# Performance work log

Hardware: AMD Instinct MI355X
Metric: run time of the kernel (lower is better)

The kernel has to match this reference:

```python
import jax, jax.numpy as jnp
import numpy as np

B, N, L, C, K = 2, 8192, 8192, 128, 8
RADIUS = 0.4

def _gather(t, idx):
    # t: [B,L,D], idx: [B,N,K] -> [B,N,K,D]
    b, n, k = idx.shape
    return jnp.take_along_axis(t, idx.reshape(b, n * k)[:, :, None], axis=1).reshape(b, n, k, t.shape[-1])

def _ln(x, g, b):
    m = x.mean(-1, keepdims=True)
    v = x.var(-1, keepdims=True)
    return (x - m) * jax.lax.rsqrt(v + 1e-5) * g + b

def setup_inputs() -> dict:
    key = jax.random.key(0)
    ks = jax.random.split(key, 16)
    F = 4 * C
    def w(k, i, o):
        return jax.random.normal(k, (i, o), jnp.float32) / np.sqrt(i).astype(np.float32)
    return {
        "q_xyz": jax.random.uniform(ks[0], (B, N, 3), jnp.float32),
        "q_feat": jax.random.normal(ks[1], (B, N, C), jnp.float32),
        "kv_xyz": jax.random.uniform(ks[2], (B, L, 3), jnp.float32),
        "kv_feat": jax.random.normal(ks[3], (B, L, C), jnp.float32),
        "kv_pad": jnp.zeros((B, L), bool),
        "pos_w1": w(ks[4], 3, C), "pos_b1": jnp.zeros((C,), jnp.float32),
        "pos_w2": w(ks[5], C, C), "pos_b2": jnp.zeros((C,), jnp.float32),
        "attn_w": w(ks[6], C, C), "attn_b": jnp.zeros((C,), jnp.float32),
        "lin_w": w(ks[7], C, C),
        "lin_src_w": w(ks[8], C, C),
        "lin_dst_w": w(ks[9], C, C),
        "ln1_g": jnp.ones((C,), jnp.float32), "ln1_b": jnp.zeros((C,), jnp.float32),
        "ffn_w1": w(ks[10], C, F), "ffn_b1": jnp.zeros((F,), jnp.float32),
        "ffn_w2": w(ks[11], F, C), "ffn_b2": jnp.zeros((C,), jnp.float32),
        "ln2_g": jnp.ones((C,), jnp.float32), "ln2_b": jnp.zeros((C,), jnp.float32),
    }

def reference(q_xyz, q_feat, kv_xyz, kv_feat, kv_pad,
              pos_w1, pos_b1, pos_w2, pos_b2, attn_w, attn_b,
              lin_w, lin_src_w, lin_dst_w, ln1_g, ln1_b,
              ffn_w1, ffn_b1, ffn_w2, ffn_b2, ln2_g, ln2_b):
    # --- radius graph: up to K nearest kv points within RADIUS per query ---
    d2 = jnp.sum((q_xyz[:, :, None, :] - kv_xyz[:, None, :, :]) ** 2, -1)  # [B,N,L]
    ok = (d2 <= RADIUS ** 2) & (~kv_pad)[:, None, :]
    neg_d2, idx = jax.lax.top_k(jnp.where(ok, -d2, -jnp.inf), K)  # [B,N,K]
    ev = jnp.isfinite(neg_d2)  # edge-valid mask [B,N,K]

    # --- PointTransformerConv (vector attention, per-edge) ---
    pos_j = _gather(kv_xyz, idx)                           # [B,N,K,3]
    rel = q_xyz[:, :, None, :] - pos_j                     # pos_i - pos_j
    # pos_nn: MLP([3,C,C], plain_last=False) => ReLU after each Linear
    delta = jax.nn.relu(jax.nn.relu(rel @ pos_w1 + pos_b1) @ pos_w2 + pos_b2)  # [B,N,K,C]
    a_src = _gather(kv_feat @ lin_src_w, idx)              # [B,N,K,C]
    a_dst = q_feat @ lin_dst_w                             # [B,N,C]
    x_j = _gather(kv_feat @ lin_w, idx)                    # [B,N,K,C]
    # attn_nn: MLP([C,C], plain_last=False) => Linear + ReLU
    alpha = jax.nn.relu((a_dst[:, :, None, :] - a_src + delta) @ attn_w + attn_b)
    # segment softmax over the K neighbors (invalid edges masked out)
    scores = jnp.where(ev[..., None], alpha, -jnp.inf)
    mx = jnp.max(scores, axis=2, keepdims=True)
    mx = jnp.where(jnp.isfinite(mx), mx, 0.0)
    e = jnp.where(ev[..., None], jnp.exp(scores - mx), 0.0)
    attn = e / jnp.maximum(e.sum(2, keepdims=True), 1e-12)
    agg = jnp.sum(attn * (x_j + delta), axis=2)            # [B,N,C]

    # --- residual + LN + FFN + LN (dropout = identity at eval) ---
    out = _ln(q_feat + agg, ln1_g, ln1_b)
    h = jax.nn.gelu(out @ ffn_w1 + ffn_b1, approximate=False) @ ffn_w2 + ffn_b2
    return _ln(out + h, ln2_g, ln2_b)
```

## Files before the change

kernel.cpp:

```cpp
#include <hip/hip_runtime.h>
#include <math.h>

#define NB 2
#define NQ 8192
#define NL 8192
#define NC 128
#define NKN 8
#define NF 512
#define MQ (NB*NQ)

typedef __attribute__((ext_vector_type(8))) short bf16x8;
typedef __attribute__((ext_vector_type(4))) float f32x4;

__device__ __forceinline__ unsigned short f2bf_u(float f){
    unsigned u = __float_as_uint(f);
    return (unsigned short)((u + 0x7FFFu + ((u>>16)&1u)) >> 16);
}
__device__ __forceinline__ float bf2f(unsigned short s){
    return __uint_as_float(((unsigned)s) << 16);
}


__global__ __launch_bounds__(256) void grid_zero_kernel(int* __restrict__ p)
{
    int t = blockIdx.x*256 + threadIdx.x;
    p[t] = 0;
}

__device__ __forceinline__ int cell_coord(float x) {
    int c = (int)(x * 16.0f);
    return min(15, max(0, c));
}

__global__ __launch_bounds__(256) void grid_count_kernel(
    const float* __restrict__ kxyz, const unsigned char* __restrict__ pad,
    int* __restrict__ cnt)
{
    int t = blockIdx.x*256 + threadIdx.x;
    if (pad[t]) return;
    int bat = t >> 13;
    float x = kxyz[t*3+0], y = kxyz[t*3+1], z = kxyz[t*3+2];
    int cell = (cell_coord(z)*16 + cell_coord(y))*16 + cell_coord(x);
    atomicAdd(&cnt[bat*4096 + cell], 1);
}

__global__ __launch_bounds__(1024) void grid_scan_kernel(
    const int* __restrict__ cnt, int* __restrict__ cs)
{
    __shared__ int wsum[17];
    int t = threadIdx.x;
    int v[8]; int s = 0;
    #pragma unroll
    for (int k = 0; k < 8; ++k) { v[k] = s; s += cnt[t*8 + k]; }
    int lane = t & 63, w = t >> 6;
    int inc = s;
    #pragma unroll
    for (int d = 1; d < 64; d <<= 1) {
        int o = __shfl_up(inc, d);
        if (lane >= d) inc += o;
    }
    if (lane == 63) wsum[w] = inc;
    __syncthreads();
    if (t == 0) {
        int a = 0;
        for (int i = 0; i < 16; ++i) { int x = wsum[i]; wsum[i] = a; a += x; }
        wsum[16] = a;
    }
    __syncthreads();
    int base = wsum[w] + (inc - s);
    #pragma unroll
    for (int k = 0; k < 8; ++k) cs[t*8 + k] = base + v[k];
    if (t == 1023) cs[8192] = wsum[16];
}

__global__ __launch_bounds__(256) void grid_scatter_kernel(
    const float* __restrict__ kxyz, const unsigned char* __restrict__ pad,
    const int* __restrict__ cs, int* __restrict__ fill, float4* __restrict__ ro)
{
    int t = blockIdx.x*256 + threadIdx.x;
    if (pad[t]) return;
    int bat = t >> 13, i = t & 8191;
    float x = kxyz[t*3+0], y = kxyz[t*3+1], z = kxyz[t*3+2];
    int cell = bat*4096 + (cell_coord(z)*16 + cell_coord(y))*16 + cell_coord(x);
    int pos = cs[cell] + atomicAdd(&fill[cell], 1);
    ro[pos] = make_float4(x, y, z, __int_as_float(i));
}

__device__ __forceinline__ void insert8(float cd, int id, float dk[8], int ik[8]) {
    if (cd < dk[7]) {
        dk[7] = cd; ik[7] = id;
        #pragma unroll
        for (int r = 6; r >= 0; --r) {
            bool sw = dk[r+1] < dk[r];
            float td = dk[r]; int ti = ik[r];
            dk[r]   = sw ? dk[r+1] : dk[r];
            ik[r]   = sw ? ik[r+1] : ik[r];
            dk[r+1] = sw ? td : dk[r+1];
            ik[r+1] = sw ? ti : ik[r+1];
        }
    }
}

template<int W>
__device__ __forceinline__ void scan_block(int l, int cx, int cy, int cz,
    float qx, float qy, float qz, const int* __restrict__ CS,
    const float4* __restrict__ RO, float dk[8], int ik[8])
{
    const int D = 2*W + 1;
    int xs = max(0, cx - W), xe = min(15, cx + W);
    int nx = xe - xs + 1;
    for (int r = l; r < D*D; r += 8) {
        int dz = r / D - W, dy = r % D - W;
        int zz = cz + dz, yy = cy + dy;
        if ((unsigned)zz > 15u || (unsigned)yy > 15u) continue;
        int c0 = (zz*16 + yy)*16 + xs;
        int s = CS[c0], e = CS[c0 + nx];
        for (int p = s; p < e; ++p) {
            float4 v = RO[p];
            float dx = qx - v.x, dyv = qy - v.y, dzv = qz - v.z;
            float cd = dx*dx + dyv*dyv + dzv*dzv;
            insert8(cd, __float_as_int(v.w), dk, ik);
        }
    }
}

__device__ __forceinline__ void merge8(float dk[8], int ik[8]) {
    #pragma unroll
    for (int m = 1; m <= 4; m <<= 1) {
        float od[8]; int oi[8];
        #pragma unroll
        for (int r = 0; r < 8; ++r) {
            od[r] = __shfl_xor(dk[r], m);
            oi[r] = __shfl_xor(ik[r], m);
        }
        float nd[8]; int ni[8];
        #pragma unroll
        for (int r = 0; r < 8; ++r) {
            bool take = od[7-r] < dk[r];
            nd[r] = take ? od[7-r] : dk[r];
            ni[r] = take ? oi[7-r] : ik[r];
        }
        #pragma unroll
        for (int st = 4; st >= 1; st >>= 1) {
            #pragma unroll
            for (int r = 0; r < 8; ++r) {
                if ((r & st) == 0 && (r | st) < 8) {
                    int b = r | st;
                    bool sw = nd[b] < nd[r];
                    float td = nd[r]; int ti = ni[r];
                    nd[r] = sw ? nd[b] : nd[r];
                    ni[r] = sw ? ni[b] : ni[r];
                    nd[b] = sw ? td : nd[b];
                    ni[b] = sw ? ti : ni[b];
                }
            }
        }
        #pragma unroll
        for (int r = 0; r < 8; ++r) { dk[r] = nd[r]; ik[r] = ni[r]; }
    }
}

__global__ __launch_bounds__(256) void radius_grid_query_kernel(
    const float* __restrict__ qxyz, const int* __restrict__ cellstart,
    const float4* __restrict__ reorder, int* __restrict__ idxout)
{
    const int tid  = threadIdx.x;
    const int l    = tid & 7;
    const int qloc = tid >> 3;
    const int gq   = blockIdx.x*32 + qloc;
    const int bat  = gq >> 13;
    const float qx = qxyz[gq*3+0], qy = qxyz[gq*3+1], qz = qxyz[gq*3+2];
    const int cx = cell_coord(qx), cy = cell_coord(qy), cz = cell_coord(qz);
    const int* CS = cellstart + bat*4096;
    const float R2  = (float)(0.4*0.4);
    const float R2P = __uint_as_float(__float_as_uint(R2) + 1u);

    float dk[8]; int ik[8];
    #pragma unroll
    for (int r = 0; r < 8; ++r) { dk[r] = R2P; ik[r] = -1; }

    scan_block<2>(l, cx, cy, cz, qx, qy, qz, CS, reorder, dk, ik);
    merge8(dk, ik);
    bool done = dk[7] <= 0.015625f;

    if (!done) {
        #pragma unroll
        for (int r = 0; r < 8; ++r) { dk[r] = R2P; ik[r] = -1; }
        scan_block<4>(l, cx, cy, cz, qx, qy, qz, CS, reorder, dk, ik);
        merge8(dk, ik);
        done = dk[7] <= 0.0625f;
    }
    if (!done) {
        #pragma unroll
        for (int r = 0; r < 8; ++r) { dk[r] = R2P; ik[r] = -1; }
        scan_block<16>(l, cx, cy, cz, qx, qy, qz, CS, reorder, dk, ik);
        merge8(dk, ik);
    }

    if (l == 0) {
        int o[8];
        #pragma unroll
        for (int r = 0; r < 8; ++r) o[r] = (dk[r] <= R2) ? ik[r] : -1;
        int4 a = {o[0], o[1], o[2], o[3]};
        int4 b = {o[4], o[5], o[6], o[7]};
        *(int4*)&idxout[(size_t)gq*8 + 0] = a;
        *(int4*)&idxout[(size_t)gq*8 + 4] = b;
    }
}

__global__ __launch_bounds__(256) void prep_all_kernel(
    const float* __restrict__ posw2, const float* __restrict__ attnw,
    const float* __restrict__ lin_w, const float* __restrict__ lin_src_w,
    const float* __restrict__ lin_dst_w,
    const float* __restrict__ ffn_w1, const float* __restrict__ ffn_w2,
    unsigned short* __restrict__ imgb)
{
    int t = blockIdx.x*256 + threadIdx.x;
    if (t < 16384) {
        int k = t >> 7, n = t & 127;
        imgb[(k >> 5)*4096 + n*32 + (k & 31)] = f2bf_u(posw2[t]);
    } else if (t < 32768) {
        int u = t - 16384;
        int k = u >> 7, n = u & 127;
        imgb[16384 + (k >> 5)*4096 + n*32 + (k & 31)] = f2bf_u(attnw[u]);
    } else if (t < 65536) {
        int u = t - 32768;
        int k = u >> 8, n = u & 255;
        float v = (n < 128) ? lin_w[k*128 + n] : lin_src_w[k*128 + (n-128)];
        imgb[32768 + ((k >> 5)*256 + n)*32 + (k & 31)] = f2bf_u(v);
    } else if (t < 81920) {
        int u = t - 65536;
        int k = u >> 7, n = u & 127;
        imgb[65536 + ((k >> 5)*128 + n)*32 + (k & 31)] = f2bf_u(lin_dst_w[u]);
    } else if (t < 147456) {
        int u = t - 81920;
        int k = u >> 9, n = u & 511;
        imgb[81920 + ((k >> 5)*512 + n)*32 + (k & 31)] = f2bf_u(ffn_w1[u]);
    } else {
        int u = t - 147456;
        int k = u >> 7, n = u & 127;
        imgb[147456 + ((k >> 5)*128 + n)*32 + (k & 31)] = f2bf_u(ffn_w2[u]);
    }
}

__device__ inline float gelu_exact(float x) {
    return 0.5f*x*(1.0f + erff(x*0.7071067811865476f));
}

template<int ACT, bool OUTBF>
__global__ __launch_bounds__(256) void gemm_mfma(
    const float* __restrict__ A, const unsigned short* __restrict__ Bimg,
    const float* __restrict__ bias, void* __restrict__ outv,
    int Kd, int Nd)
{
    __shared__ unsigned short sA[64*32];
    __shared__ unsigned short sB[128*32];
    const int tid = threadIdx.x;
    const int w = tid >> 6, lane = tid & 63, l15 = lane & 15, quad = lane >> 4;
    const int row0 = blockIdx.x*64, col0 = blockIdx.y*128;

    f32x4 acc[8];
    #pragma unroll
    for (int t=0;t<8;t++){ acc[t][0]=0.f; acc[t][1]=0.f; acc[t][2]=0.f; acc[t][3]=0.f; }

    const int nch = Kd >> 5;
    for (int kc = 0; kc < nch; ++kc) {
        __syncthreads();
        #pragma unroll
        for (int it = 0; it < 2; ++it) {
            int idx = it*256 + tid;
            int r = idx >> 3, kq = idx & 7;
            float4 a4 = *(const float4*)&A[(size_t)(row0+r)*Kd + kc*32 + kq*4];
            ushort4 pk = { f2bf_u(a4.x), f2bf_u(a4.y), f2bf_u(a4.z), f2bf_u(a4.w) };
            *(ushort4*)&sA[r*32 + kq*4] = pk;
        }
        const int4* bsrc = (const int4*)(Bimg + ((size_t)kc*Nd + col0)*32);
        #pragma unroll
        for (int it = 0; it < 2; ++it) {
            int o = it*256 + tid;
            ((int4*)sB)[o] = bsrc[o];
        }
        __syncthreads();
        bf16x8 af = *(const bf16x8*)&sA[(w*16 + l15)*32 + quad*8];
        #pragma unroll
        for (int t = 0; t < 8; ++t) {
            bf16x8 bf = *(const bf16x8*)&sB[(16*t + l15)*32 + quad*8];
            acc[t] = __builtin_amdgcn_mfma_f32_16x16x32_bf16(af, bf, acc[t], 0, 0, 0);
        }
    }

    const int rowb = row0 + w*16 + quad*4;
    #pragma unroll
    for (int t = 0; t < 8; ++t) {
        int col = col0 + 16*t + l15;
        float bv = bias ? bias[col] : 0.f;
        #pragma unroll
        for (int r = 0; r < 4; ++r) {
            float x = acc[t][r] + bv;
            if (ACT == 1) x = gelu_exact(x);
            if (OUTBF) ((unsigned short*)outv)[(size_t)(rowb+r)*Nd + col] = f2bf_u(x);
            else       ((float*)outv)[(size_t)(rowb+r)*Nd + col] = x;
        }
    }
}

__global__ __launch_bounds__(256) void gemm2_ln_mfma(
    const unsigned short* __restrict__ Abf, const unsigned short* __restrict__ Bimg,
    const float* __restrict__ b2, const float* __restrict__ res,
    const float* __restrict__ g, const float* __restrict__ bb,
    float* __restrict__ out)
{
    __shared__ unsigned short sA[64*32];
    __shared__ unsigned short sB[128*32];
    const int tid = threadIdx.x;
    const int w = tid >> 6, lane = tid & 63, l15 = lane & 15, quad = lane >> 4;
    const int row0 = blockIdx.x*64;

    f32x4 acc[8];
    #pragma unroll
    for (int t=0;t<8;t++){ acc[t][0]=0.f; acc[t][1]=0.f; acc[t][2]=0.f; acc[t][3]=0.f; }

    for (int kc = 0; kc < 16; ++kc) {
        __syncthreads();
        {
            int r = tid >> 2, kq = tid & 3;
            ((int4*)sA)[tid] = *(const int4*)&Abf[(size_t)(row0+r)*NF + kc*32 + kq*8];
        }
        const int4* bsrc = (const int4*)(Bimg + (size_t)kc*NC*32);
        #pragma unroll
        for (int it = 0; it < 2; ++it) {
            int o = it*256 + tid;
            ((int4*)sB)[o] = bsrc[o];
        }
        __syncthreads();
        bf16x8 af = *(const bf16x8*)&sA[(w*16 + l15)*32 + quad*8];
        #pragma unroll
        for (int t = 0; t < 8; ++t) {
            bf16x8 bf = *(const bf16x8*)&sB[(16*t + l15)*32 + quad*8];
            acc[t] = __builtin_amdgcn_mfma_f32_16x16x32_bf16(af, bf, acc[t], 0, 0, 0);
        }
    }

    const int rowb = row0 + w*16 + quad*4;
    #pragma unroll
    for (int r = 0; r < 4; ++r) {
        int row = rowb + r;
        float xv[8]; float S = 0.f;
        #pragma unroll
        for (int t = 0; t < 8; ++t) {
            int col = 16*t + l15;
            xv[t] = acc[t][r] + b2[col] + res[(size_t)row*NC + col];
            S += xv[t];
        }
        #pragma unroll
        for (int m = 1; m <= 8; m <<= 1) S += __shfl_xor(S, m);
        float mean = S * (1.f/128.f);
        float V = 0.f;
        #pragma unroll
        for (int t = 0; t < 8; ++t) { float d = xv[t]-mean; V += d*d; }
        #pragma unroll
        for (int m = 1; m <= 8; m <<= 1) V += __shfl_xor(V, m);
        float rstd = rsqrtf(V*(1.f/128.f) + 1e-5f);
        #pragma unroll
        for (int t = 0; t < 8; ++t) {
            int col = 16*t + l15;
            out[(size_t)row*NC + col] = (xv[t]-mean)*rstd*g[col] + bb[col];
        }
    }
}

__global__ __launch_bounds__(256) void attn_mfma_kernel(
    const float* __restrict__ qxyz, const float* __restrict__ qfeat,
    const float* __restrict__ kxyz,
    const float* __restrict__ posw1, const float* __restrict__ posb1,
    const float* __restrict__ posb2, const float* __restrict__ attnb,
    const float* __restrict__ ln1g, const float* __restrict__ ln1b,
    const unsigned short* __restrict__ wimg1, const unsigned short* __restrict__ wimg2,
    const int* __restrict__ idx, const unsigned short* __restrict__ vs,
    const float* __restrict__ adst, float* __restrict__ out1)
{
    __shared__ unsigned short s_w[16384];
    __shared__ unsigned short s_V[4*16*136];
    __shared__ unsigned short s_T[4*16*136];
    __shared__ float s_w1[384];
    __shared__ float s_b1[128], s_b2[128], s_ab[128], s_g[128], s_bb[128];
    __shared__ int   s_j[64];

    const int tid  = threadIdx.x;
    const int w    = tid >> 6;
    const int lane = tid & 63;
    const int l15  = lane & 15;
    const int quad = lane >> 4;
    const int qbase = blockIdx.x*8 + w*2;
    const int bat  = (blockIdx.x*8) >> 13;

    if (tid < 128) {
        s_b1[tid] = posb1[tid]; s_b2[tid] = posb2[tid];
        s_ab[tid] = attnb[tid]; s_g[tid] = ln1g[tid]; s_bb[tid] = ln1b[tid];
    } else {
        int i = tid - 128;
        s_w1[i] = posw1[i]; s_w1[128+i] = posw1[128+i]; s_w1[256+i] = posw1[256+i];
    }
    if (tid < 64) s_j[tid] = idx[(size_t)blockIdx.x*64 + tid];
    #pragma unroll
    for (int r = 0; r < 8; ++r)
        ((int4*)s_w)[r*256 + tid] = ((const int4*)wimg1)[r*256 + tid];
    __syncthreads();

    #pragma unroll
    for (int i = 0; i < 4; ++i) {
        int ix = lane + i*64;
        int el = ix >> 4, c16 = ix & 15;
        int j = s_j[w*16 + el];
        int jc = j < 0 ? 0 : j;
        const int4* rp = (const int4*)(vs + ((size_t)(bat*NL + jc))*256);
        int dst = (w*16 + el)*136 + c16*8;
        *(int4*)&s_V[dst] = rp[c16];
        *(int4*)&s_T[dst] = rp[16 + c16];
    }

    bf16x8 h1f[4];
    {
        int e  = w*16 + l15;
        int qh = qbase + (l15 >> 3);
        int j  = s_j[e];
        int jc = j < 0 ? 0 : j;
        const float* kp = kxyz + ((size_t)(bat*NL + jc))*3;
        float rx = qxyz[qh*3+0]-kp[0], ry = qxyz[qh*3+1]-kp[1], rz = qxyz[qh*3+2]-kp[2];
        #pragma unroll
        for (int kk=0;kk<4;kk++){
            #pragma unroll
            for (int jj=0;jj<8;jj++){
                int c = kk*32 + quad*8 + jj;
                float h = s_b1[c] + rx*s_w1[c] + ry*s_w1[128+c] + rz*s_w1[256+c];
                h = fmaxf(h, 0.f);
                h1f[kk][jj] = (short)f2bf_u(h);
            }
        }
    }

    f32x4 acc[8];
    #pragma unroll
    for (int t=0;t<8;t++){ acc[t][0]=0.f; acc[t][1]=0.f; acc[t][2]=0.f; acc[t][3]=0.f; }
    #pragma unroll
    for (int kk=0;kk<4;kk++){
        #pragma unroll
        for (int t=0;t<8;t++){
            bf16x8 wf = *(const bf16x8*)&s_w[kk*4096 + (16*t + l15)*32 + quad*8];
            acc[t] = __builtin_amdgcn_mfma_f32_16x16x32_bf16(h1f[kk], wf, acc[t], 0, 0, 0);
        }
    }

    f32x4 dreg[8];
    #pragma unroll
    for (int t=0;t<8;t++){
        float b2v = s_b2[16*t + l15];
        #pragma unroll
        for (int r=0;r<4;r++) dreg[t][r] = fmaxf(acc[t][r] + b2v, 0.f);
    }

    int jr[4]; bool val[4];
    #pragma unroll
    for (int r=0;r<4;r++){
        int j = s_j[w*16 + quad*4 + r];
        val[r] = (j >= 0); jr[r] = j < 0 ? 0 : j;
    }
    const int qt = qbase + (quad >> 1);
    float ad[8];
    #pragma unroll
    for (int t=0;t<8;t++) ad[t] = adst[(size_t)qt*NC + 16*t + l15];

    __syncthreads();

    #pragma unroll
    for (int r = 0; r < 8; ++r)
        ((int4*)s_w)[r*256 + tid] = ((const int4*)wimg2)[r*256 + tid];

    {
        unsigned short* st = s_T + w*16*136;
        #pragma unroll
        for (int t=0;t<8;t++){
            #pragma unroll
            for (int r=0;r<4;r++){
                int o = (quad*4 + r)*136 + 16*t + l15;
                float sv = bf2f(st[o]);
                st[o] = f2bf_u(ad[t] - sv + dreg[t][r]);
            }
        }
    }
    __syncthreads();

    f32x4 acc2[8];
    #pragma unroll
    for (int t=0;t<8;t++){ acc2[t][0]=0.f; acc2[t][1]=0.f; acc2[t][2]=0.f; acc2[t][3]=0.f; }
    {
        const unsigned short* st = s_T + w*16*136;
        #pragma unroll
        for (int kk=0;kk<4;kk++){
            bf16x8 tf = *(const bf16x8*)&st[l15*136 + kk*32 + quad*8];
            #pragma unroll
            for (int t=0;t<8;t++){
                bf16x8 wf = *(const bf16x8*)&s_w[kk*4096 + (16*t + l15)*32 + quad*8];
                acc2[t] = __builtin_amdgcn_mfma_f32_16x16x32_bf16(tf, wf, acc2[t], 0, 0, 0);
            }
        }
    }

    float ex[8][4]; float dnm[8];
    #pragma unroll
    for (int t=0;t<8;t++){
        float ab = s_ab[16*t + l15];
        float s0 = val[0] ? fmaxf(acc2[t][0] + ab, 0.f) : -INFINITY;
        float s1 = val[1] ? fmaxf(acc2[t][1] + ab, 0.f) : -INFINITY;
        float s2 = val[2] ? fmaxf(acc2[t][2] + ab, 0.f) : -INFINITY;
        float s3 = val[3] ? fmaxf(acc2[t][3] + ab, 0.f) : -INFINITY;
        float mx = fmaxf(fmaxf(s0,s1), fmaxf(s2,s3));
        mx = fmaxf(mx, __shfl_xor(mx, 16));
        if (mx < -1e37f) mx = 0.f;
        ex[t][0] = __expf(s0 - mx);
        ex[t][1] = __expf(s1 - mx);
        ex[t][2] = __expf(s2 - mx);
        ex[t][3] = __expf(s3 - mx);
        float sm = ex[t][0]+ex[t][1]+ex[t][2]+ex[t][3];
        sm += __shfl_xor(sm, 16);
        dnm[t] = fmaxf(sm, 1e-12f);
    }

    float part[8];
    #pragma unroll
    for (int t=0;t<8;t++){
        float p = 0.f;
        #pragma unroll
        for (int r=0;r<4;r++){
            float vv = bf2f(s_V[(w*16 + quad*4 + r)*136 + 16*t + l15]);
            p += ex[t][r] * (vv + dreg[t][r]);
        }
        p += __shfl_xor(p, 16);
        part[t] = p / dnm[t];
    }

    float xln[8];
    float S = 0.f;
    #pragma unroll
    for (int t=0;t<8;t++){
        xln[t] = qfeat[(size_t)qt*NC + 16*t + l15] + part[t];
        S += xln[t];
    }
    #pragma unroll
    for (int m=1;m<=8;m<<=1) S += __shfl_xor(S, m);
    float mean = S * (1.f/128.f);
    float V = 0.f;
    #pragma unroll
    for (int t=0;t<8;t++){ float d = xln[t]-mean; V += d*d; }
    #pragma unroll
    for (int m=1;m<=8;m<<=1) V += __shfl_xor(V, m);
    float rstd = rsqrtf(V*(1.f/128.f) + 1e-5f);

    if ((quad & 1) == 0){
        #pragma unroll
        for (int t=0;t<8;t++){
            int c = 16*t + l15;
            out1[(size_t)qt*NC + c] = (xln[t]-mean)*rstd*s_g[c] + s_bb[c];
        }
    }
}

extern "C" void kernel_launch(void* const* d_in, const int* in_sizes, int n_in,
                              void* d_out, int out_size, void* d_ws, size_t ws_size,
                              hipStream_t stream)
{
    (void)in_sizes; (void)n_in; (void)out_size; (void)ws_size;
    const float* q_xyz   = (const float*)d_in[0];
    const float* q_feat  = (const float*)d_in[1];
    const float* kv_xyz  = (const float*)d_in[2];
    const float* kv_feat = (const float*)d_in[3];
    const unsigned char* kv_pad = (const unsigned char*)d_in[4];
    const float* pos_w1  = (const float*)d_in[5];
    const float* pos_b1  = (const float*)d_in[6];
    const float* pos_w2  = (const float*)d_in[7];
    const float* pos_b2  = (const float*)d_in[8];
    const float* attn_w  = (const float*)d_in[9];
    const float* attn_b  = (const float*)d_in[10];
    const float* lin_w   = (const float*)d_in[11];
    const float* lin_src_w = (const float*)d_in[12];
    const float* lin_dst_w = (const float*)d_in[13];
    const float* ln1_g   = (const float*)d_in[14];
    const float* ln1_b   = (const float*)d_in[15];
    const float* ffn_w1  = (const float*)d_in[16];
    const float* ffn_b1  = (const float*)d_in[17];
    const float* ffn_w2  = (const float*)d_in[18];
    const float* ffn_b2  = (const float*)d_in[19];
    const float* ln2_g   = (const float*)d_in[20];
    const float* ln2_b   = (const float*)d_in[21];

    float* ws    = (float*)d_ws;
    int*   idx   = (int*)d_ws;
    unsigned short* vs = (unsigned short*)(ws + 131072);
    float* adst  = ws + 131072 + 2*2097152;
    float* out1  = adst + 2097152;
    float* Hreg  = out1 + 2097152;
    unsigned short* Hbuf = (unsigned short*)Hreg;

    float4* reorder  = (float4*)Hreg;
    int* cellcnt   = (int*)(reorder + 16384);
    int* cellfill  = cellcnt + 8192;
    int* cellstart = cellfill + 8192;

    unsigned short* imgb  = (unsigned short*)((char*)Hreg + 18u*1024*1024);
    unsigned short* wimg1 = imgb;
    unsigned short* wimg2 = imgb + 16384;
    unsigned short* wvs   = imgb + 32768;
    unsigned short* wd    = imgb + 65536;
    unsigned short* wf1   = imgb + 81920;
    unsigned short* wf2   = imgb + 147456;

    prep_all_kernel<<<dim3(832), dim3(256), 0, stream>>>(
        pos_w2, attn_w, lin_w, lin_src_w, lin_dst_w, ffn_w1, ffn_w2, imgb);

    grid_zero_kernel<<<dim3(64), dim3(256), 0, stream>>>(cellcnt);
    grid_count_kernel<<<dim3(64), dim3(256), 0, stream>>>(kv_xyz, kv_pad, cellcnt);
    grid_scan_kernel<<<dim3(1), dim3(1024), 0, stream>>>(cellcnt, cellstart);
    grid_scatter_kernel<<<dim3(64), dim3(256), 0, stream>>>(kv_xyz, kv_pad, cellstart, cellfill, reorder);
    radius_grid_query_kernel<<<dim3(MQ/32), dim3(256), 0, stream>>>(q_xyz, cellstart, reorder, idx);

    gemm_mfma<0,true ><<<dim3(MQ/64,2), dim3(256), 0, stream>>>(kv_feat, wvs, nullptr, vs,   128, 256);
    gemm_mfma<0,false><<<dim3(MQ/64,1), dim3(256), 0, stream>>>(q_feat,  wd,  nullptr, adst, 128, 128);

    attn_mfma_kernel<<<dim3(MQ/8), dim3(256), 0, stream>>>(
        q_xyz, q_feat, kv_xyz,
        pos_w1, pos_b1, pos_b2, attn_b, ln1_g, ln1_b,
        wimg1, wimg2, idx, vs, adst, out1);

    gemm_mfma<1,true ><<<dim3(MQ/64,4), dim3(256), 0, stream>>>(out1, wf1, ffn_b1, Hbuf, 128, 512);
    gemm2_ln_mfma<<<dim3(MQ/64), dim3(256), 0, stream>>>(Hbuf, wf2, ffn_b2, out1, ln2_g, ln2_b, (float*)d_out);
}
```

Measured before the change: 234.2 us.

## Fuse FFN into one kernel, merge linear GEMMs, fold grid zeroing into prep

The FFN up-projection with GELU and the down-projection with LayerNorm now run in one kernel, and the hidden activations stay in shared memory per wave instead of making a bf16 round trip through global memory. The two input projection GEMMs are merged into a single launch with a three-column grid, and cell-count zeroing moves into the weight prep kernel. Together these cut several kernel launches and a 16 MB intermediate buffer. The cost is that the fused FFN reads weights directly from global memory/L2 without LDS staging, and it uses smaller 128-thread blocks.

```diff
diff --git a/kernel.cpp b/kernel.cpp
--- a/kernel.cpp
+++ b/kernel.cpp
@@ -20,12 +20,6 @@
     return __uint_as_float(((unsigned)s) << 16);
 }
 
-
-__global__ __launch_bounds__(256) void grid_zero_kernel(int* __restrict__ p)
-{
-    int t = blockIdx.x*256 + threadIdx.x;
-    p[t] = 0;
-}
 
 __device__ __forceinline__ int cell_coord(float x) {
     int c = (int)(x * 16.0f);
@@ -213,7 +207,7 @@
     const float* __restrict__ lin_w, const float* __restrict__ lin_src_w,
     const float* __restrict__ lin_dst_w,
     const float* __restrict__ ffn_w1, const float* __restrict__ ffn_w2,
-    unsigned short* __restrict__ imgb)
+    unsigned short* __restrict__ imgb, int* __restrict__ zero_p)
 {
     int t = blockIdx.x*256 + threadIdx.x;
     if (t < 16384) {
@@ -236,97 +230,46 @@
         int u = t - 81920;
         int k = u >> 9, n = u & 511;
         imgb[81920 + ((k >> 5)*512 + n)*32 + (k & 31)] = f2bf_u(ffn_w1[u]);
-    } else {
+    } else if (t < 212992) {
         int u = t - 147456;
         int k = u >> 7, n = u & 127;
         imgb[147456 + ((k >> 5)*128 + n)*32 + (k & 31)] = f2bf_u(ffn_w2[u]);
-    }
-}
-
-__device__ inline float gelu_exact(float x) {
-    return 0.5f*x*(1.0f + erff(x*0.7071067811865476f));
-}
-
-template<int ACT, bool OUTBF>
-__global__ __launch_bounds__(256) void gemm_mfma(
-    const float* __restrict__ A, const unsigned short* __restrict__ Bimg,
-    const float* __restrict__ bias, void* __restrict__ outv,
-    int Kd, int Nd)
-{
-    __shared__ unsigned short sA[64*32];
-    __shared__ unsigned short sB[128*32];
-    const int tid = threadIdx.x;
-    const int w = tid >> 6, lane = tid & 63, l15 = lane & 15, quad = lane >> 4;
-    const int row0 = blockIdx.x*64, col0 = blockIdx.y*128;
-
-    f32x4 acc[8];
-    #pragma unroll
-    for (int t=0;t<8;t++){ acc[t][0]=0.f; acc[t][1]=0.f; acc[t][2]=0.f; acc[t][3]=0.f; }
-
-    const int nch = Kd >> 5;
-    for (int kc = 0; kc < nch; ++kc) {
-        __syncthreads();
-        #pragma unroll
-        for (int it = 0; it < 2; ++it) {
-            int idx = it*256 + tid;
-            int r = idx >> 3, kq = idx & 7;
-            float4 a4 = *(const float4*)&A[(size_t)(row0+r)*Kd + kc*32 + kq*4];
-            ushort4 pk = { f2bf_u(a4.x), f2bf_u(a4.y), f2bf_u(a4.z), f2bf_u(a4.w) };
-            *(ushort4*)&sA[r*32 + kq*4] = pk;
-        }
-        const int4* bsrc = (const int4*)(Bimg + ((size_t)kc*Nd + col0)*32);
-        #pragma unroll
-        for (int it = 0; it < 2; ++it) {
-            int o = it*256 + tid;
-            ((int4*)sB)[o] = bsrc[o];
-        }
-        __syncthreads();
-        bf16x8 af = *(const bf16x8*)&sA[(w*16 + l15)*32 + quad*8];
-        #pragma unroll
-        for (int t = 0; t < 8; ++t) {
-            bf16x8 bf = *(const bf16x8*)&sB[(16*t + l15)*32 + quad*8];
-            acc[t] = __builtin_amdgcn_mfma_f32_16x16x32_bf16(af, bf, acc[t], 0, 0, 0);
-        }
-    }
-
-    const int rowb = row0 + w*16 + quad*4;
-    #pragma unroll
-    for (int t = 0; t < 8; ++t) {
-        int col = col0 + 16*t + l15;
-        float bv = bias ? bias[col] : 0.f;
-        #pragma unroll
-        for (int r = 0; r < 4; ++r) {
-            float x = acc[t][r] + bv;
-            if (ACT == 1) x = gelu_exact(x);
-            if (OUTBF) ((unsigned short*)outv)[(size_t)(rowb+r)*Nd + col] = f2bf_u(x);
-            else       ((float*)outv)[(size_t)(rowb+r)*Nd + col] = x;
-        }
-    }
-}
-
-__global__ __launch_bounds__(256) void gemm2_ln_mfma(
-    const unsigned short* __restrict__ Abf, const unsigned short* __restrict__ Bimg,
-    const float* __restrict__ b2, const float* __restrict__ res,
-    const float* __restrict__ g, const float* __restrict__ bb,
-    float* __restrict__ out)
+    } else {
+        zero_p[t - 212992] = 0;
+    }
+}
+
+__global__ __launch_bounds__(256) void lin3_kernel(
+    const float* __restrict__ kv_feat, const float* __restrict__ q_feat,
+    const unsigned short* __restrict__ wvs, const unsigned short* __restrict__ wd,
+    unsigned short* __restrict__ vs, float* __restrict__ adst)
 {
     __shared__ unsigned short sA[64*32];
     __shared__ unsigned short sB[128*32];
     const int tid = threadIdx.x;
     const int w = tid >> 6, lane = tid & 63, l15 = lane & 15, quad = lane >> 4;
     const int row0 = blockIdx.x*64;
+    const int y = blockIdx.y;
+    const float* A = (y == 2) ? q_feat : kv_feat;
+    const unsigned short* Bimg = (y == 2) ? wd : wvs;
+    const int BNd = (y == 2) ? 128 : 256;
+    const int col0 = (y == 2) ? 0 : y*128;
 
     f32x4 acc[8];
     #pragma unroll
     for (int t=0;t<8;t++){ acc[t][0]=0.f; acc[t][1]=0.f; acc[t][2]=0.f; acc[t][3]=0.f; }
 
-    for (int kc = 0; kc < 16; ++kc) {
+    for (int kc = 0; kc < 4; ++kc) {
         __syncthreads();
-        {
-            int r = tid >> 2, kq = tid & 3;
-            ((int4*)sA)[tid] = *(const int4*)&Abf[(size_t)(row0+r)*NF + kc*32 + kq*8];
-        }
-        const int4* bsrc = (const int4*)(Bimg + (size_t)kc*NC*32);
+        #pragma unroll
+        for (int it = 0; it < 2; ++it) {
+            int ix = it*256 + tid;
+            int r = ix >> 3, kq = ix & 7;
+            float4 a4 = *(const float4*)&A[(size_t)(row0+r)*NC + kc*32 + kq*4];
+            ushort4 pk = { f2bf_u(a4.x), f2bf_u(a4.y), f2bf_u(a4.z), f2bf_u(a4.w) };
+            *(ushort4*)&sA[r*32 + kq*4] = pk;
+        }
+        const int4* bsrc = (const int4*)(Bimg + ((size_t)kc*BNd + col0)*32);
         #pragma unroll
         for (int it = 0; it < 2; ++it) {
             int o = it*256 + tid;
@@ -343,13 +286,99 @@
 
     const int rowb = row0 + w*16 + quad*4;
     #pragma unroll
+    for (int t = 0; t < 8; ++t) {
+        int col = col0 + 16*t + l15;
+        #pragma unroll
+        for (int r = 0; r < 4; ++r) {
+            if (y == 2) adst[(size_t)(rowb+r)*NC + col] = acc[t][r];
+            else        vs[(size_t)(rowb+r)*256 + col] = f2bf_u(acc[t][r]);
+        }
+    }
+}
+
+__device__ inline float gelu_exact(float x) {
+    return 0.5f*x*(1.0f + erff(x*0.7071067811865476f));
+}
+
+__global__ __launch_bounds__(128) void ffn_fused_kernel(
+    const float* __restrict__ in1,
+    const unsigned short* __restrict__ wf1, const unsigned short* __restrict__ wf2,
+    const float* __restrict__ b1v, const float* __restrict__ b2v,
+    const float* __restrict__ g, const float* __restrict__ bb,
+    float* __restrict__ out)
+{
+    __shared__ unsigned short sA[32*136];
+    __shared__ unsigned short sH[2*16*136];
+    const int tid = threadIdx.x;
+    const int w = tid >> 6, lane = tid & 63, l15 = lane & 15, quad = lane >> 4;
+    const int row0 = blockIdx.x*32;
+
+    #pragma unroll
+    for (int it = 0; it < 8; ++it) {
+        int ix = it*128 + tid;
+        int r = ix >> 5, kq = ix & 31;
+        float4 a4 = *(const float4*)&in1[(size_t)(row0+r)*NC + kq*4];
+        ushort4 pk = { f2bf_u(a4.x), f2bf_u(a4.y), f2bf_u(a4.z), f2bf_u(a4.w) };
+        *(ushort4*)&sA[r*136 + kq*4] = pk;
+    }
+    __syncthreads();
+
+    bf16x8 af[4];
+    #pragma unroll
+    for (int kk=0;kk<4;kk++)
+        af[kk] = *(const bf16x8*)&sA[(w*16 + l15)*136 + kk*32 + quad*8];
+
+    f32x4 acc2[8];
+    #pragma unroll
+    for (int t=0;t<8;t++){ acc2[t][0]=0.f; acc2[t][1]=0.f; acc2[t][2]=0.f; acc2[t][3]=0.f; }
+
+    unsigned short* Hw = sH + w*16*136;
+
+    #pragma unroll
+    for (int c = 0; c < 4; ++c) {
+        f32x4 acc1[8];
+        #pragma unroll
+        for (int t=0;t<8;t++){ acc1[t][0]=0.f; acc1[t][1]=0.f; acc1[t][2]=0.f; acc1[t][3]=0.f; }
+        #pragma unroll
+        for (int kk=0;kk<4;kk++){
+            #pragma unroll
+            for (int t=0;t<8;t++){
+                int n = c*128 + 16*t + l15;
+                bf16x8 bf = *(const bf16x8*)&wf1[((size_t)kk*512 + n)*32 + quad*8];
+                acc1[t] = __builtin_amdgcn_mfma_f32_16x16x32_bf16(af[kk], bf, acc1[t], 0, 0, 0);
+            }
+        }
+        #pragma unroll
+        for (int t=0;t<8;t++){
+            float bv = b1v[c*128 + 16*t + l15];
+            #pragma unroll
+            for (int r=0;r<4;r++){
+                float x = gelu_exact(acc1[t][r] + bv);
+                Hw[(quad*4+r)*136 + 16*t + l15] = f2bf_u(x);
+            }
+        }
+        __syncthreads();
+        #pragma unroll
+        for (int kk=0;kk<4;kk++){
+            bf16x8 a2 = *(const bf16x8*)&Hw[l15*136 + kk*32 + quad*8];
+            #pragma unroll
+            for (int t=0;t<8;t++){
+                bf16x8 bf = *(const bf16x8*)&wf2[((size_t)((c*4+kk)*128) + 16*t + l15)*32 + quad*8];
+                acc2[t] = __builtin_amdgcn_mfma_f32_16x16x32_bf16(a2, bf, acc2[t], 0, 0, 0);
+            }
+        }
+        __syncthreads();
+    }
+
+    const int rowb = row0 + w*16 + quad*4;
+    #pragma unroll
     for (int r = 0; r < 4; ++r) {
         int row = rowb + r;
         float xv[8]; float S = 0.f;
         #pragma unroll
         for (int t = 0; t < 8; ++t) {
             int col = 16*t + l15;
-            xv[t] = acc[t][r] + b2[col] + res[(size_t)row*NC + col];
+            xv[t] = acc2[t][r] + b2v[col] + in1[(size_t)row*NC + col];
             S += xv[t];
         }
         #pragma unroll
@@ -599,14 +628,13 @@
     float* adst  = ws + 131072 + 2*2097152;
     float* out1  = adst + 2097152;
     float* Hreg  = out1 + 2097152;
-    unsigned short* Hbuf = (unsigned short*)Hreg;
 
     float4* reorder  = (float4*)Hreg;
     int* cellcnt   = (int*)(reorder + 16384);
     int* cellfill  = cellcnt + 8192;
     int* cellstart = cellfill + 8192;
 
-    unsigned short* imgb  = (unsigned short*)((char*)Hreg + 18u*1024*1024);
+    unsigned short* imgb  = (unsigned short*)((char*)Hreg + (1u << 20));
     unsigned short* wimg1 = imgb;
     unsigned short* wimg2 = imgb + 16384;
     unsigned short* wvs   = imgb + 32768;
@@ -614,23 +642,21 @@
     unsigned short* wf1   = imgb + 81920;
     unsigned short* wf2   = imgb + 147456;
 
-    prep_all_kernel<<<dim3(832), dim3(256), 0, stream>>>(
-        pos_w2, attn_w, lin_w, lin_src_w, lin_dst_w, ffn_w1, ffn_w2, imgb);
-
-    grid_zero_kernel<<<dim3(64), dim3(256), 0, stream>>>(cellcnt);
+    prep_all_kernel<<<dim3(896), dim3(256), 0, stream>>>(
+        pos_w2, attn_w, lin_w, lin_src_w, lin_dst_w, ffn_w1, ffn_w2, imgb, cellcnt);
+
     grid_count_kernel<<<dim3(64), dim3(256), 0, stream>>>(kv_xyz, kv_pad, cellcnt);
     grid_scan_kernel<<<dim3(1), dim3(1024), 0, stream>>>(cellcnt, cellstart);
     grid_scatter_kernel<<<dim3(64), dim3(256), 0, stream>>>(kv_xyz, kv_pad, cellstart, cellfill, reorder);
     radius_grid_query_kernel<<<dim3(MQ/32), dim3(256), 0, stream>>>(q_xyz, cellstart, reorder, idx);
 
-    gemm_mfma<0,true ><<<dim3(MQ/64,2), dim3(256), 0, stream>>>(kv_feat, wvs, nullptr, vs,   128, 256);
-    gemm_mfma<0,false><<<dim3(MQ/64,1), dim3(256), 0, stream>>>(q_feat,  wd,  nullptr, adst, 128, 128);
+    lin3_kernel<<<dim3(MQ/64, 3), dim3(256), 0, stream>>>(kv_feat, q_feat, wvs, wd, vs, adst);
 
     attn_mfma_kernel<<<dim3(MQ/8), dim3(256), 0, stream>>>(
         q_xyz, q_feat, kv_xyz,
         pos_w1, pos_b1, pos_b2, attn_b, ln1_g, ln1_b,
         wimg1, wimg2, idx, vs, adst, out1);
 
-    gemm_mfma<1,true ><<<dim3(MQ/64,4), dim3(256), 0, stream>>>(out1, wf1, ffn_b1, Hbuf, 128, 512);
-    gemm2_ln_mfma<<<dim3(MQ/64), dim3(256), 0, stream>>>(Hbuf, wf2, ffn_b2, out1, ln2_g, ln2_b, (float*)d_out);
-}
+    ffn_fused_kernel<<<dim3(MQ/32), dim3(128), 0, stream>>>(
+        out1, wf1, wf2, ffn_b1, ffn_b2, ln2_g, ln2_b, (float*)d_out);
+}
```

Measured after the change: 261.6 us. 1.12x slower.
